# Kernel optimization log

Measured on AMD Instinct MI355X. Metric: run time of the kernel, lower is better.

## Reference

```python
import jax, jax.numpy as jnp
import numpy as np


def setup_inputs() -> dict:
    key = jax.random.key(0)
    k1, k2, k3 = jax.random.split(key, 3)
    b_n, f_num, N = 2, 4, 50
    n = b_n * f_num
    C_in, C = 256, 64
    h, w = 200, 336
    return {
        "x": jax.random.normal(k1, (n, C, h * w), jnp.float32),
        "idx_feat": jax.random.normal(k2, (n, C_in, N, 1), jnp.float32),
        "weight": jax.random.normal(k3, (C, C_in), jnp.float32) * 0.01,
        "bias": jnp.zeros((C,), jnp.float32),
        "thing_gt_idx": jnp.ones((b_n, N, f_num), jnp.int32),
        "h": h,
        "w": w,
    }


def _con_loss(mw, b_n, N, f_num, C):
    # mw: (b_n*f_num, C, N, 1) kernel embeddings after embed_extractor
    K = N * f_num
    # reshape/permute mirrors torch: (b_n, N, f_num, C) flattened row-major ->
    # rows ordered (instance, frame), matching the boolean-mask gather order
    # under a dense (all-ones) thing_gt_idx mask.
    m = mw.reshape(b_n, f_num, C, N).transpose(0, 3, 1, 2).reshape(b_n, K, C)
    # F.normalize(dim=1)
    m = m / jnp.maximum(jnp.linalg.norm(m, axis=-1, keepdims=True), 1e-12)
    sim = jnp.einsum('bkc,blc->bkl', m, m)  # (b_n, K, K)
    labels = np.repeat(np.arange(N), f_num)  # instance id per row (static)
    f_own = np.tile(np.arange(f_num), N)     # frame id per row (static)
    # static negative gather indices: all columns of other instances, padded by
    # repeating the last negative (torch's while-loop torch.cat) to length K-1
    neg_cols = []
    for i in range(N):
        cols = np.nonzero(labels != i)[0]
        neg_cols.append(np.concatenate([cols, np.full(f_num - 1, cols[-1])]))
    neg_idx = np.stack(neg_cols)[labels]     # (K, K-1)
    # random positive among the f_num-1 same-instance / other-frame entries
    r = jax.random.randint(jax.random.key(42), (b_n, K), 0, f_num - 1)
    pos_off = jnp.where(r >= f_own[None, :], r + 1, r)
    pos_col = labels[None, :] * f_num + pos_off  # (b_n, K)
    positives = sim[jnp.arange(b_n)[:, None], jnp.arange(K)[None, :], pos_col]
    negatives = sim[:, np.arange(K)[:, None], neg_idx]  # (b_n, K, K-1)
    logits = jnp.concatenate([positives[..., None], negatives], axis=-1) / 0.07
    # CrossEntropyLoss with target 0, mean over K rows, summed over batches
    lse = jax.scipy.special.logsumexp(logits, axis=-1)
    return jnp.sum(jnp.mean(lse - logits[..., 0], axis=-1))


def reference(x, idx_feat, weight, bias, thing_gt_idx, h, w):
    b_n, N, f_num = thing_gt_idx.shape
    n = b_n * f_num
    C = weight.shape[0]
    # embed_extractor: 1x1 conv == channel matmul
    mw = jnp.einsum('bcnk,dc->bdnk', idx_feat, weight) + bias[None, :, None, None]
    loss = _con_loss(mw, b_n, N, f_num, C)
    # shuffle_times == 1 branch: kernels @ encoded features
    kernels = mw.reshape(n, C, N).transpose(0, 2, 1)  # (n, N, C)
    inst_pred = jnp.matmul(kernels, x).reshape(n, N, h, w)
    return inst_pred, loss
```

## Files before the change

### kernel.cpp

```cpp
#include <hip/hip_runtime.h>
#include <stdint.h>
#include <float.h>
#include <math.h>

#define HW_TOT 67200
#define NBF 8
#define CO 64
#define CI 256
#define NN 50
#define KK 200
#define BN 2

__device__ __forceinline__ uint32_t rotl32(uint32_t v, int n) {
  return (v << n) | (v >> (32 - n));
}

__device__ void tf2x32(uint32_t k0, uint32_t k1, uint32_t x0, uint32_t x1,
                       uint32_t& o0, uint32_t& o1) {
  const uint32_t ks2 = k0 ^ k1 ^ 0x1BD11BDAu;
  x0 += k0; x1 += k1;
  x0 += x1; x1 = rotl32(x1, 13); x1 ^= x0;
  x0 += x1; x1 = rotl32(x1, 15); x1 ^= x0;
  x0 += x1; x1 = rotl32(x1, 26); x1 ^= x0;
  x0 += x1; x1 = rotl32(x1, 6);  x1 ^= x0;
  x0 += k1; x1 += ks2 + 1u;
  x0 += x1; x1 = rotl32(x1, 17); x1 ^= x0;
  x0 += x1; x1 = rotl32(x1, 29); x1 ^= x0;
  x0 += x1; x1 = rotl32(x1, 16); x1 ^= x0;
  x0 += x1; x1 = rotl32(x1, 24); x1 ^= x0;
  x0 += ks2; x1 += k0 + 2u;
  x0 += x1; x1 = rotl32(x1, 13); x1 ^= x0;
  x0 += x1; x1 = rotl32(x1, 15); x1 ^= x0;
  x0 += x1; x1 = rotl32(x1, 26); x1 ^= x0;
  x0 += x1; x1 = rotl32(x1, 6);  x1 ^= x0;
  x0 += k0; x1 += k1 + 3u;
  x0 += x1; x1 = rotl32(x1, 17); x1 ^= x0;
  x0 += x1; x1 = rotl32(x1, 29); x1 ^= x0;
  x0 += x1; x1 = rotl32(x1, 16); x1 ^= x0;
  x0 += x1; x1 = rotl32(x1, 24); x1 ^= x0;
  x0 += k1; x1 += ks2 + 4u;
  x0 += x1; x1 = rotl32(x1, 13); x1 ^= x0;
  x0 += x1; x1 = rotl32(x1, 15); x1 ^= x0;
  x0 += x1; x1 = rotl32(x1, 26); x1 ^= x0;
  x0 += x1; x1 = rotl32(x1, 6);  x1 ^= x0;
  o0 = x0 + ks2;
  o1 = x1 + k0 + 5u;
}

__device__ int jax_r(int b, int k) {
  uint32_t k1a, k1b, k2a, k2b, h0, h1, l0, l1;
  tf2x32(0u, 42u, 0u, 0u, k1a, k1b);
  tf2x32(0u, 42u, 0u, 1u, k2a, k2b);
  const uint32_t idx = (uint32_t)(b * KK + k);
  tf2x32(k1a, k1b, 0u, idx, h0, h1);
  tf2x32(k2a, k2b, 0u, idx, l0, l1);
  const uint32_t hb = h0 ^ h1, lb = l0 ^ l1;
  return (int)(((hb % 3u) + (lb % 3u)) % 3u);
}

__global__ __launch_bounds__(256) void k_mw(const float* __restrict__ idx_feat,
                                            const float* __restrict__ weight,
                                            const float* __restrict__ bias,
                                            float* __restrict__ mw) {
  const int tid = blockIdx.x * 256 + threadIdx.x;
  if (tid >= NBF * CO * NN) return;
  const int n = tid % NN;
  const int rest = tid / NN;
  const int d = rest % CO;
  const int b = rest / CO;
  float acc = bias[d];
  const float* feat = idx_feat + (size_t)(b * CI) * NN + n;
  const float* wrow = weight + d * CI;
  #pragma unroll 8
  for (int ci = 0; ci < CI; ++ci)
    acc = fmaf(feat[ci * NN], wrow[ci], acc);
  mw[tid] = acc;
}

__device__ __forceinline__ float waveMax(float v) {
  #pragma unroll
  for (int o = 32; o > 0; o >>= 1) v = fmaxf(v, __shfl_down(v, o));
  return v;
}
__device__ __forceinline__ float waveSum(float v) {
  #pragma unroll
  for (int o = 32; o > 0; o >>= 1) v += __shfl_down(v, o);
  return v;
}

__global__ __launch_bounds__(256) void k_loss(const float* __restrict__ mw,
                                              float* __restrict__ partial) {
  __shared__ __align__(16) float m_lds[KK][68];
  __shared__ float red[8];
  __shared__ float pos_sh;
  __shared__ int rvals[32];

  const int b = blockIdx.x >> 3;
  const int chunk = blockIdx.x & 7;
  const int t = threadIdx.x;
  const int wid = t >> 6, lane = t & 63;
  const int kbase = chunk * 25;

  if (t < 25) rvals[t] = jax_r(b, kbase + t);

  float row[CO];
  if (t < KK) {
    const int f = t & 3, ni = t >> 2;
    const float* src = mw + (size_t)((b * 4 + f) * CO) * NN + ni;
    float ssq = 0.f;
    #pragma unroll
    for (int c = 0; c < CO; ++c) { const float v = src[c * NN]; row[c] = v; ssq += v * v; }
    const float inv = 1.0f / fmaxf(sqrtf(ssq), 1e-12f);
    #pragma unroll
    for (int c = 0; c < CO; ++c) { row[c] *= inv; m_lds[t][c] = row[c]; }
  }
  __syncthreads();

  float part = 0.f;
  for (int kk = 0; kk < 25; ++kk) {
    const int k = kbase + kk;
    const int g = k >> 2, fo = k & 3;
    const int r = rvals[kk];
    const int pos_off = (r >= fo) ? r + 1 : r;
    const int pos_col = (g << 2) + pos_off;
    const int last_neg = (g == NN - 1) ? (KK - 5) : (KK - 1);

    float dot = 0.f;
    if (t < KK) {
      const float4* mk = reinterpret_cast<const float4*>(&m_lds[k][0]);
      #pragma unroll
      for (int c4 = 0; c4 < 16; ++c4) {
        const float4 a = mk[c4];
        dot = fmaf(a.x, row[4 * c4 + 0], dot);
        dot = fmaf(a.y, row[4 * c4 + 1], dot);
        dot = fmaf(a.z, row[4 * c4 + 2], dot);
        dot = fmaf(a.w, row[4 * c4 + 3], dot);
      }
    }
    const float logit = dot * (1.0f / 0.07f);

    float wgt = 0.f;
    if (t < KK) {
      if (t == pos_col) wgt = 1.f;
      else if ((t >> 2) != g) wgt = (t == last_neg) ? 4.f : 1.f;
    }
    const bool valid = wgt > 0.f;

    const float wmax = waveMax(valid ? logit : -FLT_MAX);
    if (lane == 0) red[wid] = wmax;
    if (t == pos_col) pos_sh = logit;
    __syncthreads();
    const float mx = fmaxf(fmaxf(red[0], red[1]), fmaxf(red[2], red[3]));
    const float pos = pos_sh;
    const float ws = waveSum(valid ? wgt * expf(logit - mx) : 0.f);
    if (lane == 0) red[4 + wid] = ws;
    __syncthreads();
    if (t == 0) {
      const float s = red[4] + red[5] + red[6] + red[7];
      part += (mx + logf(s)) - pos;
    }
    __syncthreads();
  }
  if (t == 0) partial[blockIdx.x] = part;
}

typedef __attribute__((ext_vector_type(8))) short bf16x8;
typedef __attribute__((ext_vector_type(4))) float f32x4;

__device__ __forceinline__ uint32_t bf16rne(float f) {
  uint32_t u = __builtin_bit_cast(uint32_t, f);
  return (u + 0x7FFFu + ((u >> 16) & 1u)) >> 16;
}

__global__ __launch_bounds__(64, 3) void k_pred(const float* __restrict__ x,
                                                const float* __restrict__ mw,
                                                const float* __restrict__ partial,
                                                float* __restrict__ out) {
  __shared__ __align__(16) char wlds[64 * 136];

  const int b = blockIdx.y;
  const int p0 = blockIdx.x * 64;
  const int l = threadIdx.x;
  const int ln = l & 15, lg = l >> 4;

  const float* xb  = x  + (size_t)b * CO * HW_TOT + p0 + l;
  const float* mwb = mw + (size_t)b * CO * NN;

  bf16x8 afr[4][2];
  #pragma unroll
  for (int ns = 0; ns < 4; ++ns) {
    const int n = min(ns * 16 + ln, NN - 1);
    #pragma unroll
    for (int ks = 0; ks < 2; ++ks)
      #pragma unroll
      for (int j = 0; j < 8; ++j)
        afr[ns][ks][j] = (short)bf16rne(mwb[(ks * 32 + lg * 8 + j) * NN + n]);
  }

  float xr[64];
  #pragma unroll
  for (int c = 0; c < 64; ++c)
    xr[c] = xb[(size_t)c * HW_TOT];

  #pragma unroll
  for (int c = 0; c < 64; c += 2) {
    const uint32_t pk = bf16rne(xr[c]) | (bf16rne(xr[c + 1]) << 16);
    *reinterpret_cast<uint32_t*>(wlds + l * 136 + c * 2) = pk;
  }

  f32x4 acc[4][4];
  #pragma unroll
  for (int ns = 0; ns < 4; ++ns)
    #pragma unroll
    for (int q = 0; q < 4; ++q) acc[ns][q] = (f32x4){0.f, 0.f, 0.f, 0.f};

  #pragma unroll
  for (int ks = 0; ks < 2; ++ks) {
    #pragma unroll
    for (int q = 0; q < 4; ++q) {
      const bf16x8 bfr = *reinterpret_cast<const bf16x8*>(
          wlds + (q * 16 + ln) * 136 + (ks * 32 + lg * 8) * 2);
      #pragma unroll
      for (int ns = 0; ns < 4; ++ns)
        acc[ns][q] = __builtin_amdgcn_mfma_f32_16x16x32_bf16(afr[ns][ks], bfr,
                                                             acc[ns][q], 0, 0, 0);
    }
  }

  asm volatile("s_waitcnt lgkmcnt(0)" ::: "memory");
  __builtin_amdgcn_sched_barrier(0);

  float* ot = reinterpret_cast<float*>(wlds);
  float* ob = out + (size_t)b * NN * HW_TOT + p0 + l;

  #pragma unroll
  for (int half = 0; half < 2; ++half) {
    #pragma unroll
    for (int ns = 0; ns < 2; ++ns)
      #pragma unroll
      for (int q = 0; q < 4; ++q)
        #pragma unroll
        for (int i = 0; i < 4; ++i)
          ot[(ns * 16 + 4 * lg + i) * 68 + q * 16 + ln] = acc[half * 2 + ns][q][i];

    asm volatile("s_waitcnt lgkmcnt(0)" ::: "memory");
    __builtin_amdgcn_sched_barrier(0);

    #pragma unroll
    for (int r = 0; r < 32; ++r) {
      const int n = half * 32 + r;
      if (n < NN)
        __builtin_nontemporal_store(ot[r * 68 + l], ob + (size_t)n * HW_TOT);
    }

    if (half == 0) {
      asm volatile("s_waitcnt lgkmcnt(0)" ::: "memory");
      __builtin_amdgcn_sched_barrier(0);
    }
  }

  if (blockIdx.x == 0 && b == 0 && l == 0) {
    float s = 0.f;
    #pragma unroll
    for (int i = 0; i < 16; ++i) s += partial[i];
    out[(size_t)NBF * NN * HW_TOT] = s * (1.0f / KK);
  }
}

extern "C" void kernel_launch(void* const* d_in, const int* in_sizes, int n_in,
                              void* d_out, int out_size, void* d_ws, size_t ws_size,
                              hipStream_t stream) {
  const float* x        = (const float*)d_in[0];
  const float* idx_feat = (const float*)d_in[1];
  const float* weight   = (const float*)d_in[2];
  const float* bias     = (const float*)d_in[3];
  float* out = (float*)d_out;

  float* mw = (float*)d_ws;
  float* partial = mw + NBF * CO * NN;

  hipLaunchKernelGGL(k_mw, dim3((NBF * CO * NN + 255) / 256), dim3(256), 0, stream,
                     idx_feat, weight, bias, mw);
  hipLaunchKernelGGL(k_loss, dim3(16), dim3(256), 0, stream, mw, partial);
  hipLaunchKernelGGL(k_pred, dim3(HW_TOT / 64, NBF), dim3(64), 0, stream,
                     x, mw, partial, out);
}
```

Before: 85.31 us.

## Widen prediction blocks to six waves sharing LDS staging

Each k_pred block now has 384 threads (six waves) instead of a single 64-lane wave, so each block covers 384 pixels. x is loaded in groups of 16 channels to reduce register pressure, and every thread writes its bf16-packed values into a shared LDS tile. After the MFMAs, all six waves write their outputs into one LDS tile, and the block stores 25 output rows per pass with coalesced 384-wide stores. The gains sought are fewer blocks, lower VGPR use and higher occupancy; the cost is extra __syncthreads barriers and a larger LDS footprint per block.

```diff
diff --git a/kernel.cpp b/kernel.cpp
--- a/kernel.cpp
+++ b/kernel.cpp
@@ -10,6 +10,8 @@
 #define NN 50
 #define KK 200
 #define BN 2
+#define PT 384
+#define WAVES 6
 
 __device__ __forceinline__ uint32_t rotl32(uint32_t v, int n) {
   return (v << n) | (v >> (32 - n));
@@ -172,18 +174,20 @@
   return (u + 0x7FFFu + ((u >> 16) & 1u)) >> 16;
 }
 
-__global__ __launch_bounds__(64, 3) void k_pred(const float* __restrict__ x,
+__global__ __launch_bounds__(PT, 4) void k_pred(const float* __restrict__ x,
                                                 const float* __restrict__ mw,
                                                 const float* __restrict__ partial,
                                                 float* __restrict__ out) {
-  __shared__ __align__(16) char wlds[64 * 136];
+  __shared__ __align__(16) char lds[PT * 136];
 
   const int b = blockIdx.y;
-  const int p0 = blockIdx.x * 64;
-  const int l = threadIdx.x;
+  const int pbase = blockIdx.x * PT;
+  const int u = threadIdx.x;
+  const int l = u & 63;
+  const int w = u >> 6;
   const int ln = l & 15, lg = l >> 4;
 
-  const float* xb  = x  + (size_t)b * CO * HW_TOT + p0 + l;
+  const float* xb  = x  + (size_t)b * CO * HW_TOT + pbase;
   const float* mwb = mw + (size_t)b * CO * NN;
 
   bf16x8 afr[4][2];
@@ -197,16 +201,19 @@
         afr[ns][ks][j] = (short)bf16rne(mwb[(ks * 32 + lg * 8 + j) * NN + n]);
   }
 
-  float xr[64];
-  #pragma unroll
-  for (int c = 0; c < 64; ++c)
-    xr[c] = xb[(size_t)c * HW_TOT];
-
-  #pragma unroll
-  for (int c = 0; c < 64; c += 2) {
-    const uint32_t pk = bf16rne(xr[c]) | (bf16rne(xr[c + 1]) << 16);
-    *reinterpret_cast<uint32_t*>(wlds + l * 136 + c * 2) = pk;
-  }
+  #pragma unroll
+  for (int g = 0; g < 4; ++g) {
+    float xr[16];
+    #pragma unroll
+    for (int j = 0; j < 16; ++j)
+      xr[j] = xb[(size_t)(g * 16 + j) * HW_TOT + u];
+    #pragma unroll
+    for (int j = 0; j < 16; j += 2) {
+      const uint32_t pk = bf16rne(xr[j]) | (bf16rne(xr[j + 1]) << 16);
+      *reinterpret_cast<uint32_t*>(lds + u * 136 + (g * 16 + j) * 2) = pk;
+    }
+  }
+  __syncthreads();
 
   f32x4 acc[4][4];
   #pragma unroll
@@ -219,7 +226,7 @@
     #pragma unroll
     for (int q = 0; q < 4; ++q) {
       const bf16x8 bfr = *reinterpret_cast<const bf16x8*>(
-          wlds + (q * 16 + ln) * 136 + (ks * 32 + lg * 8) * 2);
+          lds + (size_t)(w * 64 + q * 16 + ln) * 136 + (ks * 32 + lg * 8) * 2);
       #pragma unroll
       for (int ns = 0; ns < 4; ++ns)
         acc[ns][q] = __builtin_amdgcn_mfma_f32_16x16x32_bf16(afr[ns][ks], bfr,
@@ -227,39 +234,36 @@
     }
   }
 
-  asm volatile("s_waitcnt lgkmcnt(0)" ::: "memory");
-  __builtin_amdgcn_sched_barrier(0);
-
-  float* ot = reinterpret_cast<float*>(wlds);
-  float* ob = out + (size_t)b * NN * HW_TOT + p0 + l;
+  float* olds = reinterpret_cast<float*>(lds);
+  float* ob = out + (size_t)b * NN * HW_TOT + pbase;
 
   #pragma unroll
   for (int half = 0; half < 2; ++half) {
-    #pragma unroll
-    for (int ns = 0; ns < 2; ++ns)
-      #pragma unroll
-      for (int q = 0; q < 4; ++q)
-        #pragma unroll
-        for (int i = 0; i < 4; ++i)
-          ot[(ns * 16 + 4 * lg + i) * 68 + q * 16 + ln] = acc[half * 2 + ns][q][i];
-
-    asm volatile("s_waitcnt lgkmcnt(0)" ::: "memory");
-    __builtin_amdgcn_sched_barrier(0);
-
-    #pragma unroll
-    for (int r = 0; r < 32; ++r) {
-      const int n = half * 32 + r;
+    __syncthreads();
+
+    #pragma unroll
+    for (int ns = 0; ns < 4; ++ns)
+      #pragma unroll
+      for (int i = 0; i < 4; ++i) {
+        const int n = ns * 16 + 4 * lg + i;
+        const int r = n - half * 25;
+        if (r >= 0 && r < 25 && n < NN) {
+          #pragma unroll
+          for (int q = 0; q < 4; ++q)
+            olds[r * 385 + w * 64 + q * 16 + ln] = acc[ns][q][i];
+        }
+      }
+    __syncthreads();
+
+    #pragma unroll
+    for (int r = 0; r < 25; ++r) {
+      const int n = half * 25 + r;
       if (n < NN)
-        __builtin_nontemporal_store(ot[r * 68 + l], ob + (size_t)n * HW_TOT);
-    }
-
-    if (half == 0) {
-      asm volatile("s_waitcnt lgkmcnt(0)" ::: "memory");
-      __builtin_amdgcn_sched_barrier(0);
-    }
-  }
-
-  if (blockIdx.x == 0 && b == 0 && l == 0) {
+        __builtin_nontemporal_store(olds[r * 385 + u], ob + (size_t)n * HW_TOT + u);
+    }
+  }
+
+  if (blockIdx.x == 0 && b == 0 && u == 0) {
     float s = 0.f;
     #pragma unroll
     for (int i = 0; i < 16; ++i) s += partial[i];
@@ -282,6 +286,6 @@
   hipLaunchKernelGGL(k_mw, dim3((NBF * CO * NN + 255) / 256), dim3(256), 0, stream,
                      idx_feat, weight, bias, mw);
   hipLaunchKernelGGL(k_loss, dim3(16), dim3(256), 0, stream, mw, partial);
-  hipLaunchKernelGGL(k_pred, dim3(HW_TOT / 64, NBF), dim3(64), 0, stream,
+  hipLaunchKernelGGL(k_pred, dim3(HW_TOT / PT, NBF), dim3(PT), 0, stream,
                      x, mw, partial, out);
 }
```

After: 89.50 us. +4.9%, slower.
